# Kernel optimization log

Measured on AMD Instinct MI355X. Metric: run time of the kernel, lower is better.

Reference implementation:

```python
import jax, jax.numpy as jnp
import numpy as np

K = 3        # kernel size
STRIDE = 1
PAD = 1      # k // 2


def setup_inputs() -> dict:
    key = jax.random.key(0)
    k1, k2, k3, k4 = jax.random.split(key, 4)
    B, C, H, W = 8, 128, 64, 64
    x = jax.random.normal(k1, (B, C, H, W), jnp.float32)
    offset = jax.random.normal(k2, (B, 2 * K * K, H, W), jnp.float32)
    mask = jax.random.uniform(k3, (B, K * K, H, W), jnp.float32)
    dyn_weight = jax.random.normal(k4, (B, C, K, K), jnp.float32)
    return {"x": x, "offset": offset, "mask": mask, "dyn_weight": dyn_weight}


def _deform_depthwise(img, off, msk, w):
    # img: [C,H,W], off: [2*K*K,Ho,Wo], msk: [K*K,Ho,Wo], w: [C,K,K]
    C, H, W = img.shape
    KK = K * K
    Ho = (H + 2 * PAD - K) // STRIDE + 1
    Wo = (W + 2 * PAD - K) // STRIDE + 1

    # base sampling grid per kernel tap (row-major taps, (y,x) offset pairs)
    ky, kx = jnp.meshgrid(jnp.arange(K), jnp.arange(K), indexing='ij')
    ky = ky.reshape(KK).astype(jnp.float32)
    kx = kx.reshape(KK).astype(jnp.float32)
    base_y = (jnp.arange(Ho) * STRIDE - PAD).astype(jnp.float32)
    base_x = (jnp.arange(Wo) * STRIDE - PAD).astype(jnp.float32)
    off = off.reshape(KK, 2, Ho, Wo)
    py = base_y[None, :, None] + ky[:, None, None] + off[:, 0]   # [KK,Ho,Wo]
    px = base_x[None, None, :] + kx[:, None, None] + off[:, 1]   # [KK,Ho,Wo]

    y0f = jnp.floor(py)
    x0f = jnp.floor(px)
    dy = py - y0f
    dx = px - x0f

    def gather(yf, xf):
        # zero-padded bilinear corner gather -> [C,KK,Ho,Wo]
        valid = (yf >= 0) & (yf < H) & (xf >= 0) & (xf < W)
        yi = jnp.clip(yf, 0, H - 1).astype(jnp.int32)
        xi = jnp.clip(xf, 0, W - 1).astype(jnp.int32)
        return img[:, yi, xi] * valid.astype(img.dtype)[None]

    v00 = gather(y0f, x0f)
    v01 = gather(y0f, x0f + 1)
    v10 = gather(y0f + 1, x0f)
    v11 = gather(y0f + 1, x0f + 1)

    sampled = (v00 * ((1 - dy) * (1 - dx))[None] + v01 * ((1 - dy) * dx)[None]
               + v10 * (dy * (1 - dx))[None] + v11 * (dy * dx)[None])
    modulated = sampled * msk[None]                               # [C,KK,Ho,Wo]
    return jnp.einsum('ckhw,ck->chw', modulated, w.reshape(C, KK))


def reference(x, offset, mask, dyn_weight):
    # dyn_weight path: per-sample depthwise modulated deformable conv
    # (weight [C,1,K,K] with groups=C, no bias), vmapped over batch instead
    # of the original Python loop.
    return jax.vmap(_deform_depthwise)(x, offset, mask, dyn_weight)
```

## Files before the change

### kernel.cpp

```cpp
#include <hip/hip_runtime.h>


#define BB 8
#define CC 128
#define HH 64
#define WW 64
#define HWs (HH*WW)
#define KKT 9
#define CH 16
#define NCG (CC/CH)
#define CPI 4
#define NIT (CH/CPI)
#define ROWS 4
#define NHS (HH/ROWS)
#define WLO 5
#define WR  (ROWS+12)
#define CLO 5
#define WC  74
#define CELLS (WR*WC)
#define NTHR 256
#define NK  ((CELLS + NTHR - 1)/NTHR)

__global__ __launch_bounds__(NTHR, 2)
void mdcn_kernel(const float* __restrict__ x,
                 const float* __restrict__ offset,
                 const float* __restrict__ mask,
                 const float* __restrict__ dynw,
                 float* __restrict__ out)
{
    __shared__ float4 lds[2][CELLS];

    const int blk = blockIdx.x;
    const int hs = blk & (NHS - 1);
    const int cg = (blk >> 4) & (NCG - 1);
    const int b  = blk >> 7;
    const int tid = threadIdx.x;
    const int w = tid & 63;
    const int h0 = hs * ROWS;
    const int h = h0 + (tid >> 6);

    const float* xg = x + (size_t)(b * CC + cg * CH) * HWs;

    float4 stg[NK];
    #define STAGE_LOAD(XP)                                                    \
    do {                                                                      \
        const float* xp_ = (XP);                                              \
        _Pragma("unroll")                                                     \
        for (int k = 0; k < NK; ++k) {                                        \
            const int idx = tid + k * NTHR;                                   \
            float4 v = make_float4(0.f, 0.f, 0.f, 0.f);                       \
            if (idx < CELLS) {                                                \
                const int row = idx / WC;                                     \
                const int col = idx - row * WC - CLO;                         \
                const int ar  = h0 - WLO + row;                               \
                if ((unsigned)ar < (unsigned)HH &&                            \
                    (unsigned)col < (unsigned)WW) {                           \
                    const float* pp = xp_ + ar * WW + col;                    \
                    v.x = pp[0 * HWs]; v.y = pp[1 * HWs];                     \
                    v.z = pp[2 * HWs]; v.w = pp[3 * HWs];                     \
                }                                                             \
            }                                                                 \
            stg[k] = v;                                                       \
        }                                                                     \
    } while (0)

    #define STAGE_WRITE(DST)                                                  \
    do {                                                                      \
        float4* Lb_ = &lds[DST][0];                                           \
        _Pragma("unroll")                                                     \
        for (int k = 0; k < NK; ++k) {                                        \
            const int idx = tid + k * NTHR;                                   \
            if (idx < CELLS) Lb_[idx] = stg[k];                               \
        }                                                                     \
    } while (0)

    STAGE_LOAD(xg);

    float mv[KKT], dyv[KKT], dxv[KKT];
    int   woff[KKT];
    int   badmask = 0;
    const float* offp = offset + (size_t)b * (2 * KKT) * HWs + h * WW + w;
    const float* mskp = mask   + (size_t)b * KKT * HWs       + h * WW + w;
    #pragma unroll
    for (int t = 0; t < KKT; ++t) {
        const float oy = offp[(2 * t)     * HWs];
        const float ox = offp[(2 * t + 1) * HWs];
        const float m  = mskp[t * HWs];
        const float py = (float)(h - 1 + t / 3) + oy;
        const float px = (float)(w - 1 + t % 3) + ox;
        const float fy = floorf(py), fx = floorf(px);
        const int y0 = (int)fy, x0 = (int)fx;
        dyv[t] = py - fy;
        dxv[t] = px - fx;
        const bool inwin = (y0 >= h0 - WLO) && (y0 <= h0 - WLO + WR - 2) &&
                           (x0 >= -CLO)     && (x0 <= -CLO + WC - 2);
        if (!inwin) {
            badmask |= (1 << t);
            woff[t] = 0;
            mv[t] = 0.f;
        } else {
            woff[t] = (y0 - (h0 - WLO)) * WC + (x0 + CLO);
            mv[t] = m;
        }
    }
    const int anybad = __any(badmask != 0);

    STAGE_WRITE(0);
    __syncthreads();

    const float* wtb  = dynw + (size_t)(b * CC + cg * CH) * KKT;
    float*       outp = out  + (size_t)(b * CC + cg * CH) * HWs + h * WW + w;

    for (int it = 0; it < NIT; ++it) {
        const float* wt = wtb + it * CPI * KKT;
        float s0 = 0.f, s1 = 0.f, s2 = 0.f, s3 = 0.f;

        if (anybad) {
            #pragma unroll
            for (int t = 0; t < KKT; ++t) {
                if (badmask & (1 << t)) {
                    const float oy = offp[(2 * t)     * HWs];
                    const float ox = offp[(2 * t + 1) * HWs];
                    const float m  = mskp[t * HWs];
                    const float py = (float)(h - 1 + t / 3) + oy;
                    const float px = (float)(w - 1 + t % 3) + ox;
                    const float fy = floorf(py), fx = floorf(px);
                    const float dy = py - fy, dx = px - fx;
                    const int y0 = (int)fy, x0 = (int)fx;
                    const int y1 = y0 + 1,  x1 = x0 + 1;
                    const int cy0 = min(max(y0, 0), HH - 1);
                    const int cy1 = min(max(y1, 0), HH - 1);
                    const int cx0 = min(max(x0, 0), WW - 1);
                    const int cx1 = min(max(x1, 0), WW - 1);
                    const float m00 = ((unsigned)y0 < HH && (unsigned)x0 < WW) ? 1.f : 0.f;
                    const float m01 = ((unsigned)y0 < HH && (unsigned)x1 < WW) ? 1.f : 0.f;
                    const float m10 = ((unsigned)y1 < HH && (unsigned)x0 < WW) ? 1.f : 0.f;
                    const float m11 = ((unsigned)y1 < HH && (unsigned)x1 < WW) ? 1.f : 0.f;
                    const float omdy = 1.f - dy, omdx = 1.f - dx;
                    #pragma unroll
                    for (int c = 0; c < CPI; ++c) {
                        const float* pl = xg + (size_t)(it * CPI + c) * HWs;
                        const float v = pl[cy0 * WW + cx0] * m00 * (omdy * omdx)
                                      + pl[cy0 * WW + cx1] * m01 * (omdy * dx)
                                      + pl[cy1 * WW + cx0] * m10 * (dy * omdx)
                                      + pl[cy1 * WW + cx1] * m11 * (dy * dx);
                        const float add = v * m * wt[c * KKT + t];
                        if      (c == 0) s0 += add;
                        else if (c == 1) s1 += add;
                        else if (c == 2) s2 += add;
                        else             s3 += add;
                    }
                }
            }
        }

        if (it + 1 < NIT) {
            STAGE_LOAD(xg + (size_t)(it + 1) * CPI * HWs);
        }

        const float4* Lp = &lds[it & 1][0];
        #pragma unroll
        for (int t = 0; t < KKT; ++t) {
            const float4 c00 = Lp[woff[t]];
            const float4 c01 = Lp[woff[t] + 1];
            const float4 c10 = Lp[woff[t] + WC];
            const float4 c11 = Lp[woff[t] + WC + 1];
            const float dy = dyv[t], dx = dxv[t], m = mv[t];
            const float omdy = 1.f - dy, omdx = 1.f - dx;
            const float w00 = omdy * omdx * m, w01 = omdy * dx * m;
            const float w10 = dy * omdx * m,   w11 = dy * dx * m;
            const float v0 = c00.x * w00 + c01.x * w01 + c10.x * w10 + c11.x * w11;
            const float v1 = c00.y * w00 + c01.y * w01 + c10.y * w10 + c11.y * w11;
            const float v2 = c00.z * w00 + c01.z * w01 + c10.z * w10 + c11.z * w11;
            const float v3 = c00.w * w00 + c01.w * w01 + c10.w * w10 + c11.w * w11;
            s0 += v0 * wt[0 * KKT + t];
            s1 += v1 * wt[1 * KKT + t];
            s2 += v2 * wt[2 * KKT + t];
            s3 += v3 * wt[3 * KKT + t];
        }

        if (it + 1 < NIT) {
            STAGE_WRITE((it + 1) & 1);
        }

        outp[(size_t)(it * CPI + 0) * HWs] = s0;
        outp[(size_t)(it * CPI + 1) * HWs] = s1;
        outp[(size_t)(it * CPI + 2) * HWs] = s2;
        outp[(size_t)(it * CPI + 3) * HWs] = s3;

        if (it + 1 < NIT) {
            __syncthreads();
        }
    }
    #undef STAGE_LOAD
    #undef STAGE_WRITE
}

extern "C" void kernel_launch(void* const* d_in, const int* in_sizes, int n_in,
                              void* d_out, int out_size, void* d_ws, size_t ws_size,
                              hipStream_t stream) {
    const float* x      = (const float*)d_in[0];
    const float* offset = (const float*)d_in[1];
    const float* mask   = (const float*)d_in[2];
    const float* dynw   = (const float*)d_in[3];
    float* out = (float*)d_out;

    dim3 grid(BB * NCG * NHS);
    dim3 block(NTHR);
    mdcn_kernel<<<grid, block, 0, stream>>>(x, offset, mask, dynw, out);
}
```

Baseline: 34.97 us.

## Store LDS tile as fp16 pairs with duplicated odd-shifted copy for single-load bilinear

The input tile is converted to half precision while it is staged in LDS. Each row is stored as adjacent column pairs, and a second copy is shifted by one column, so both horizontal bilinear neighbours come back in a single 16-byte load. This cuts the LDS reads per tap from four float4 loads to two. The cost is extra conversion work, twice as many LDS writes, and fp16 rounding of the input, which may break the accuracy tolerance.

New measurement: 43.50 us. 24.4% more time.

```diff
diff --git a/kernel.cpp b/kernel.cpp
--- a/kernel.cpp
+++ b/kernel.cpp
@@ -1,4 +1,5 @@
 #include <hip/hip_runtime.h>
+#include <hip/hip_fp16.h>
 
 
 #define BB 8
@@ -17,9 +18,13 @@
 #define WR  (ROWS+12)
 #define CLO 5
 #define WC  74
-#define CELLS (WR*WC)
+#define WCP 37
+#define PCELLS (WR*WCP)
+#define BUFCELLS (2*PCELLS)
+#define ODELTA (PCELLS*16)
+#define CSLOTS (WR*WC)
 #define NTHR 256
-#define NK  ((CELLS + NTHR - 1)/NTHR)
+#define NK  ((CSLOTS + NTHR - 1)/NTHR)
 
 __global__ __launch_bounds__(NTHR, 2)
 void mdcn_kernel(const float* __restrict__ x,
@@ -28,7 +33,7 @@
                  const float* __restrict__ dynw,
                  float* __restrict__ out)
 {
-    __shared__ float4 lds[2][CELLS];
+    __shared__ float4 lds[2][BUFCELLS];
 
     const int blk = blockIdx.x;
     const int hs = blk & (NHS - 1);
@@ -41,7 +46,8 @@
 
     const float* xg = x + (size_t)(b * CC + cg * CH) * HWs;
 
-    float4 stg[NK];
+    unsigned stgL[NK], stgH[NK];
+
     #define STAGE_LOAD(XP)                                                    \
     do {                                                                      \
         const float* xp_ = (XP);                                              \
@@ -49,7 +55,7 @@
         for (int k = 0; k < NK; ++k) {                                        \
             const int idx = tid + k * NTHR;                                   \
             float4 v = make_float4(0.f, 0.f, 0.f, 0.f);                       \
-            if (idx < CELLS) {                                                \
+            if (idx < CSLOTS) {                                               \
                 const int row = idx / WC;                                     \
                 const int col = idx - row * WC - CLO;                         \
                 const int ar  = h0 - WLO + row;                               \
@@ -60,17 +66,31 @@
                     v.z = pp[2 * HWs]; v.w = pp[3 * HWs];                     \
                 }                                                             \
             }                                                                 \
-            stg[k] = v;                                                       \
+            __half2 l_ = __floats2half2_rn(v.x, v.y);                         \
+            __half2 h_ = __floats2half2_rn(v.z, v.w);                         \
+            stgL[k] = *(unsigned*)&l_;                                        \
+            stgH[k] = *(unsigned*)&h_;                                        \
         }                                                                     \
     } while (0)
 
     #define STAGE_WRITE(DST)                                                  \
     do {                                                                      \
-        float4* Lb_ = &lds[DST][0];                                           \
+        char* Lb_ = (char*)&lds[DST][0];                                      \
         _Pragma("unroll")                                                     \
         for (int k = 0; k < NK; ++k) {                                        \
             const int idx = tid + k * NTHR;                                   \
-            if (idx < CELLS) Lb_[idx] = stg[k];                               \
+            if (idx < CSLOTS) {                                               \
+                const int row = idx / WC;                                     \
+                const int cw  = idx - row * WC;         \
+                const int eoff = (row * WCP + (cw >> 1)) * 16 + (cw & 1) * 8; \
+                *(uint2*)(Lb_ + eoff) = make_uint2(stgL[k], stgH[k]);         \
+                if (cw >= 1 && cw <= 72) {                                    \
+                    const int ooff = ODELTA                                   \
+                        + (row * WCP + ((cw - 1) >> 1)) * 16                  \
+                        + ((cw & 1) ^ 1) * 8;                                 \
+                    *(uint2*)(Lb_ + ooff) = make_uint2(stgL[k], stgH[k]);     \
+                }                                                             \
+            }                                                                 \
         }                                                                     \
     } while (0)
 
@@ -99,7 +119,9 @@
             woff[t] = 0;
             mv[t] = 0.f;
         } else {
-            woff[t] = (y0 - (h0 - WLO)) * WC + (x0 + CLO);
+            const int rb  = y0 - (h0 - WLO);
+            const int x0w = x0 + CLO;
+            woff[t] = (rb * WCP + (x0w >> 1)) * 16 + (x0w & 1) * ODELTA;
             mv[t] = m;
         }
     }
@@ -158,21 +180,29 @@
             STAGE_LOAD(xg + (size_t)(it + 1) * CPI * HWs);
         }
 
-        const float4* Lp = &lds[it & 1][0];
+        const char* bb = (const char*)&lds[it & 1][0];
         #pragma unroll
         for (int t = 0; t < KKT; ++t) {
-            const float4 c00 = Lp[woff[t]];
-            const float4 c01 = Lp[woff[t] + 1];
-            const float4 c10 = Lp[woff[t] + WC];
-            const float4 c11 = Lp[woff[t] + WC + 1];
+            const float4 r0 = *(const float4*)(bb + woff[t]);
+            const float4 r1 = *(const float4*)(bb + woff[t] + WCP * 16);
             const float dy = dyv[t], dx = dxv[t], m = mv[t];
             const float omdy = 1.f - dy, omdx = 1.f - dx;
             const float w00 = omdy * omdx * m, w01 = omdy * dx * m;
             const float w10 = dy * omdx * m,   w11 = dy * dx * m;
-            const float v0 = c00.x * w00 + c01.x * w01 + c10.x * w10 + c11.x * w11;
-            const float v1 = c00.y * w00 + c01.y * w01 + c10.y * w10 + c11.y * w11;
-            const float v2 = c00.z * w00 + c01.z * w01 + c10.z * w10 + c11.z * w11;
-            const float v3 = c00.w * w00 + c01.w * w01 + c10.w * w10 + c11.w * w11;
+            const __half2* p0 = (const __half2*)&r0;
+            const __half2* p1 = (const __half2*)&r1;
+            const float2 A01 = __half22float2(p0[0]);
+            const float2 A23 = __half22float2(p0[1]);
+            const float2 B01 = __half22float2(p0[2]);
+            const float2 B23 = __half22float2(p0[3]);
+            const float2 C01 = __half22float2(p1[0]);
+            const float2 C23 = __half22float2(p1[1]);
+            const float2 D01 = __half22float2(p1[2]);
+            const float2 D23 = __half22float2(p1[3]);
+            const float v0 = A01.x * w00 + B01.x * w01 + C01.x * w10 + D01.x * w11;
+            const float v1 = A01.y * w00 + B01.y * w01 + C01.y * w10 + D01.y * w11;
+            const float v2 = A23.x * w00 + B23.x * w01 + C23.x * w10 + D23.x * w11;
+            const float v3 = A23.y * w00 + B23.y * w01 + C23.y * w10 + D23.y * w11;
             s0 += v0 * wt[0 * KKT + t];
             s1 += v1 * wt[1 * KKT + t];
             s2 += v2 * wt[2 * KKT + t];
```

## Halve channel group, shrink halo window, pack per-tap state into half precision

Applied to the files above, without the earlier changes.

Channels per block drop from 16 to 8, which doubles the grid. The LDS halo window shrinks from a 5-cell margin to a 4-cell margin. Per-tap bilinear fractions are stored as packed half2 and window offsets as packed 16-bit pairs, cutting register pressure so more waves can stay resident. The trade-offs are reduced precision in the interpolation weights and more taps falling outside the window onto the slow path. Each block also redoes the offset and mask loads for fewer channels.

Result: slower. 44.86 us (+28.3%).

```diff
diff --git a/kernel.cpp b/kernel.cpp
--- a/kernel.cpp
+++ b/kernel.cpp
@@ -1,4 +1,5 @@
 #include <hip/hip_runtime.h>
+#include <hip/hip_fp16.h>
 
 
 #define BB 8
@@ -7,16 +8,16 @@
 #define WW 64
 #define HWs (HH*WW)
 #define KKT 9
-#define CH 16
+#define CH 8
 #define NCG (CC/CH)
 #define CPI 4
 #define NIT (CH/CPI)
 #define ROWS 4
 #define NHS (HH/ROWS)
-#define WLO 5
-#define WR  (ROWS+12)
-#define CLO 5
-#define WC  74
+#define WLO 4
+#define WR  (ROWS+10)
+#define CLO 4
+#define WC  72
 #define CELLS (WR*WC)
 #define NTHR 256
 #define NK  ((CELLS + NTHR - 1)/NTHR)
@@ -33,7 +34,7 @@
     const int blk = blockIdx.x;
     const int hs = blk & (NHS - 1);
     const int cg = (blk >> 4) & (NCG - 1);
-    const int b  = blk >> 7;
+    const int b  = blk >> 8;
     const int tid = threadIdx.x;
     const int w = tid & 63;
     const int h0 = hs * ROWS;
@@ -76,9 +77,10 @@
 
     STAGE_LOAD(xg);
 
-    float mv[KKT], dyv[KKT], dxv[KKT];
-    int   woff[KKT];
-    int   badmask = 0;
+    float    mv[KKT];
+    unsigned ddpk[KKT];
+    unsigned wpk[(KKT + 1) / 2];
+    int      badmask = 0;
     const float* offp = offset + (size_t)b * (2 * KKT) * HWs + h * WW + w;
     const float* mskp = mask   + (size_t)b * KKT * HWs       + h * WW + w;
     #pragma unroll
@@ -90,18 +92,22 @@
         const float px = (float)(w - 1 + t % 3) + ox;
         const float fy = floorf(py), fx = floorf(px);
         const int y0 = (int)fy, x0 = (int)fx;
-        dyv[t] = py - fy;
-        dxv[t] = px - fx;
+        const float dy = py - fy, dx = px - fx;
+        const __half2 hh = __floats2half2_rn(dy, dx);
+        ddpk[t] = *(const unsigned*)&hh;
         const bool inwin = (y0 >= h0 - WLO) && (y0 <= h0 - WLO + WR - 2) &&
                            (x0 >= -CLO)     && (x0 <= -CLO + WC - 2);
+        unsigned off16;
         if (!inwin) {
             badmask |= (1 << t);
-            woff[t] = 0;
+            off16 = 0;
             mv[t] = 0.f;
         } else {
-            woff[t] = (y0 - (h0 - WLO)) * WC + (x0 + CLO);
+            off16 = (unsigned)((y0 - (h0 - WLO)) * WC + (x0 + CLO));
             mv[t] = m;
         }
+        if (t & 1) wpk[t >> 1] |= off16 << 16;
+        else       wpk[t >> 1]  = off16;
     }
     const int anybad = __any(badmask != 0);
 
@@ -161,11 +167,14 @@
         const float4* Lp = &lds[it & 1][0];
         #pragma unroll
         for (int t = 0; t < KKT; ++t) {
-            const float4 c00 = Lp[woff[t]];
-            const float4 c01 = Lp[woff[t] + 1];
-            const float4 c10 = Lp[woff[t] + WC];
-            const float4 c11 = Lp[woff[t] + WC + 1];
-            const float dy = dyv[t], dx = dxv[t], m = mv[t];
+            const int wofft = (t & 1) ? (int)(wpk[t >> 1] >> 16)
+                                      : (int)(wpk[t >> 1] & 0xFFFFu);
+            const float4 c00 = Lp[wofft];
+            const float4 c01 = Lp[wofft + 1];
+            const float4 c10 = Lp[wofft + WC];
+            const float4 c11 = Lp[wofft + WC + 1];
+            const float2 dd = __half22float2(*(const __half2*)&ddpk[t]);
+            const float dy = dd.x, dx = dd.y, m = mv[t];
             const float omdy = 1.f - dy, omdx = 1.f - dx;
             const float w00 = omdy * omdx * m, w01 = omdy * dx * m;
             const float w10 = dy * omdx * m,   w11 = dy * dx * m;
```

## Store input tile as packed fp16 column pairs and use fdot2 bilinear

Applied to the files above, without the earlier changes.

The shared-memory tile now holds horizontally adjacent pixel pairs packed as fp16 for four channels, kept in two parity planes so any x0 reads one 16-byte cell per row. Each tap then needs two LDS reads instead of four, and the bilinear blend is done with packed fp16 dot-product instructions. The aim is to cut LDS traffic and ALU work per tap. In exchange the staging doubles the cell count with per-element converts, and the input values and bilinear weights lose precision to fp16, which may exceed tolerance.

New measurement: 78.27 us. 124% more time.

```diff
diff --git a/kernel.cpp b/kernel.cpp
--- a/kernel.cpp
+++ b/kernel.cpp
@@ -1,5 +1,7 @@
 #include <hip/hip_runtime.h>
 
+
+typedef _Float16 h2_t __attribute__((ext_vector_type(2)));
 
 #define BB 8
 #define CC 128
@@ -17,9 +19,13 @@
 #define WR  (ROWS+12)
 #define CLO 5
 #define WC  74
-#define CELLS (WR*WC)
+#define WCP 37
+#define PCELLS (WR*WCP)
+#define BUFCELLS (2*PCELLS)
+#define ROWB (WCP*16)
+#define ODELTA_B (PCELLS*16)
 #define NTHR 256
-#define NK  ((CELLS + NTHR - 1)/NTHR)
+#define NK  ((BUFCELLS + NTHR - 1)/NTHR)
 
 __global__ __launch_bounds__(NTHR, 2)
 void mdcn_kernel(const float* __restrict__ x,
@@ -28,7 +34,7 @@
                  const float* __restrict__ dynw,
                  float* __restrict__ out)
 {
-    __shared__ float4 lds[2][CELLS];
+    __shared__ float4 lds[2][BUFCELLS];
 
     const int blk = blockIdx.x;
     const int hs = blk & (NHS - 1);
@@ -48,19 +54,27 @@
         _Pragma("unroll")                                                     \
         for (int k = 0; k < NK; ++k) {                                        \
             const int idx = tid + k * NTHR;                                   \
-            float4 v = make_float4(0.f, 0.f, 0.f, 0.f);                       \
-            if (idx < CELLS) {                                                \
-                const int row = idx / WC;                                     \
-                const int col = idx - row * WC - CLO;                         \
+            float4 cell = make_float4(0.f, 0.f, 0.f, 0.f);                    \
+            if (idx < BUFCELLS) {                                             \
+                const int p   = (idx >= PCELLS);                              \
+                const int rem = idx - p * PCELLS;                             \
+                const int row = rem / WCP;                                    \
+                const int j   = rem - row * WCP;                              \
                 const int ar  = h0 - WLO + row;                               \
-                if ((unsigned)ar < (unsigned)HH &&                            \
-                    (unsigned)col < (unsigned)WW) {                           \
-                    const float* pp = xp_ + ar * WW + col;                    \
-                    v.x = pp[0 * HWs]; v.y = pp[1 * HWs];                     \
-                    v.z = pp[2 * HWs]; v.w = pp[3 * HWs];                     \
+                const int ca  = 2 * j + p - CLO;                              \
+                const bool rok = (unsigned)ar < (unsigned)HH;                 \
+                const bool aok = rok && (unsigned)ca < (unsigned)WW;          \
+                const bool bok = rok && (unsigned)(ca + 1) < (unsigned)WW;    \
+                const float* pr = xp_ + ar * WW;                              \
+                _Pragma("unroll")                                             \
+                for (int c = 0; c < CPI; ++c) {                               \
+                    const float fA = aok ? pr[c * HWs + ca]     : 0.f;        \
+                    const float fB = bok ? pr[c * HWs + ca + 1] : 0.f;        \
+                    h2_t hp; hp.x = (_Float16)fA; hp.y = (_Float16)fB;        \
+                    ((h2_t*)&cell)[c] = hp;                                   \
                 }                                                             \
             }                                                                 \
-            stg[k] = v;                                                       \
+            stg[k] = cell;                                                    \
         }                                                                     \
     } while (0)
 
@@ -70,7 +84,7 @@
         _Pragma("unroll")                                                     \
         for (int k = 0; k < NK; ++k) {                                        \
             const int idx = tid + k * NTHR;                                   \
-            if (idx < CELLS) Lb_[idx] = stg[k];                               \
+            if (idx < BUFCELLS) Lb_[idx] = stg[k];                            \
         }                                                                     \
     } while (0)
 
@@ -99,7 +113,10 @@
             woff[t] = 0;
             mv[t] = 0.f;
         } else {
-            woff[t] = (y0 - (h0 - WLO)) * WC + (x0 + CLO);
+            const int rb  = y0 - (h0 - WLO);
+            const int x0w = x0 + CLO;
+            woff[t] = ((x0w & 1) ? ODELTA_B : 0)
+                    + (rb * WCP + (x0w >> 1)) * 16;
             mv[t] = m;
         }
     }
@@ -158,21 +175,29 @@
             STAGE_LOAD(xg + (size_t)(it + 1) * CPI * HWs);
         }
 
-        const float4* Lp = &lds[it & 1][0];
+        const char* bb = (const char*)&lds[it & 1][0];
         #pragma unroll
         for (int t = 0; t < KKT; ++t) {
-            const float4 c00 = Lp[woff[t]];
-            const float4 c01 = Lp[woff[t] + 1];
-            const float4 c10 = Lp[woff[t] + WC];
-            const float4 c11 = Lp[woff[t] + WC + 1];
+            const float4 r0 = *(const float4*)(bb + woff[t]);
+            const float4 r1 = *(const float4*)(bb + woff[t] + ROWB);
             const float dy = dyv[t], dx = dxv[t], m = mv[t];
             const float omdy = 1.f - dy, omdx = 1.f - dx;
             const float w00 = omdy * omdx * m, w01 = omdy * dx * m;
             const float w10 = dy * omdx * m,   w11 = dy * dx * m;
-            const float v0 = c00.x * w00 + c01.x * w01 + c10.x * w10 + c11.x * w11;
-            const float v1 = c00.y * w00 + c01.y * w01 + c10.y * w10 + c11.y * w11;
-            const float v2 = c00.z * w00 + c01.z * w01 + c10.z * w10 + c11.z * w11;
-            const float v3 = c00.w * w00 + c01.w * w01 + c10.w * w10 + c11.w * w11;
+            const auto pk0 = __builtin_amdgcn_cvt_pkrtz(w00, w01);
+            const auto pk1 = __builtin_amdgcn_cvt_pkrtz(w10, w11);
+            const h2_t hw0 = __builtin_bit_cast(h2_t, pk0);
+            const h2_t hw1 = __builtin_bit_cast(h2_t, pk1);
+            const h2_t* p0 = (const h2_t*)&r0;
+            const h2_t* p1 = (const h2_t*)&r1;
+            const float v0 = __builtin_amdgcn_fdot2(p0[0], hw0,
+                               __builtin_amdgcn_fdot2(p1[0], hw1, 0.f, false), false);
+            const float v1 = __builtin_amdgcn_fdot2(p0[1], hw0,
+                               __builtin_amdgcn_fdot2(p1[1], hw1, 0.f, false), false);
+            const float v2 = __builtin_amdgcn_fdot2(p0[2], hw0,
+                               __builtin_amdgcn_fdot2(p1[2], hw1, 0.f, false), false);
+            const float v3 = __builtin_amdgcn_fdot2(p0[3], hw0,
+                               __builtin_amdgcn_fdot2(p1[3], hw1, 0.f, false), false);
             s0 += v0 * wt[0 * KKT + t];
             s1 += v1 * wt[1 * KKT + t];
             s2 += v2 * wt[2 * KKT + t];
```
